# Performance work log

Hardware: AMD Instinct MI355X
Metric: run time of the kernel (lower is better)

The kernel has to match this reference:

```python
import jax, jax.numpy as jnp
import numpy as np

N_NODES = 100000
N_EDGES = 1600000
IN_DIM, HID_DIM, OUT_DIM = 256, 128, 32
NEG_SLOPE = 0.2  # GATConv default negative_slope


def setup_inputs() -> dict:
    key = jax.random.key(0)
    ks = jax.random.split(key, 6)
    x = jax.random.normal(ks[0], (N_NODES, IN_DIM), dtype=jnp.float32)
    edge_index = jax.random.randint(ks[1], (2, N_EDGES), 0, N_NODES, dtype=jnp.int64)
    # conv1: lin_src [in, hid], att_src/att_dst [hid] (heads=1)
    W1 = jax.random.normal(ks[2], (IN_DIM, HID_DIM), dtype=jnp.float32) * 0.05
    a1_src = jax.random.normal(ks[3], (HID_DIM,), dtype=jnp.float32) * 0.05
    a1_dst = jax.random.normal(ks[4], (HID_DIM,), dtype=jnp.float32) * 0.05
    # conv2: lin_src [hid, out]; conv2 runs with attention=False so no att params needed
    W2 = jax.random.normal(ks[5], (HID_DIM, OUT_DIM), dtype=jnp.float32) * 0.05
    return {"x": x, "W1": W1, "a1_src": a1_src, "a1_dst": a1_dst, "W2": W2,
            "edge_index": edge_index}


def _gat_aggregate(xs, alpha_src, alpha_dst, src, dst, n):
    """Segment-softmax attention aggregation (heads=1).
    xs: [N,C] transformed features; alpha_src/alpha_dst: [N] per-node logits.
    Edge e: j=src[e] -> i=dst[e]; softmax over edges grouped by dst."""
    e = jax.nn.leaky_relu(alpha_src[src] + alpha_dst[dst], NEG_SLOPE)  # [E]
    m = jax.ops.segment_max(e, dst, num_segments=n)                    # [N]
    w = jnp.exp(e - m[dst])                                            # [E]
    s = jax.ops.segment_sum(w, dst, num_segments=n)                    # [N]
    a = w / s[dst]                                                     # [E]
    return jax.ops.segment_sum(xs[src] * a[:, None], dst, num_segments=n)


def reference(x, W1, a1_src, a1_dst, W2, edge_index):
    src, dst = edge_index[0], edge_index[1]
    n = x.shape[0]

    # conv1 (attention=True): also caches per-node attention logits (tied later)
    xs1 = x @ W1                       # [N, hid]
    as1 = xs1 @ a1_src                 # [N]
    ad1 = xs1 @ a1_dst                 # [N]
    h1 = jax.nn.elu(_gat_aggregate(xs1, as1, ad1, src, dst, n))

    # conv2 (attention=False): returns x @ lin_src (heads=1, concat=False)
    h2 = h1 @ W2                       # [N, out]

    # conv3: weights tied to W2^T, attention tied to conv1's logits
    xs3 = h2 @ W2.T                    # [N, hid]
    h3 = jax.nn.elu(_gat_aggregate(xs3, as1, ad1, src, dst, n))

    # conv4 (attention=False): weights tied to W1^T
    h4 = h3 @ W1.T                     # [N, in]

    return (h2, h4)
```

## Files before the change

kernel.cpp:

```cpp
#include <hip/hip_runtime.h>
#include <math.h>

#define IN_DIM 256
#define HID 128
#define OUTD 32
#define NEG_SLOPE 0.2f
#define BSH 8
#define EPB 4096

typedef unsigned short ushort_t;
typedef unsigned int uint_t;
typedef __attribute__((ext_vector_type(8))) short short8;
typedef __attribute__((ext_vector_type(4))) float f32x4;

__device__ __forceinline__ ushort_t f2b(float f) {
    union { float f; uint_t i; } v; v.f = f;
    uint_t x = v.i;
    uint_t r = (x + 0x7FFFu + ((x >> 16) & 1u)) >> 16;
    return (ushort_t)r;
}

__device__ __forceinline__ float b2f(ushort_t b) {
    union { uint_t i; float f; } v; v.i = ((uint_t)b) << 16;
    return v.f;
}

__global__ __launch_bounds__(256) void swz_kernel(
    const float* __restrict__ W1, const float* __restrict__ W2,
    ushort_t* __restrict__ W1B, ushort_t* __restrict__ W1TB, ushort_t* __restrict__ W2TB)
{
    int idx = blockIdx.x * 256 + threadIdx.x;
    if (idx < 32768) {
        int j = idx & 7, l = (idx >> 3) & 63, t = (idx >> 9) & 7, s = idx >> 12;
        int n = 16 * t + (l & 15), k = 32 * s + (l >> 4) * 8 + j;
        W1B[idx] = f2b(W1[k * HID + n]);
    } else if (idx < 65536) {
        int o = idx - 32768;
        int j = o & 7, l = (o >> 3) & 63, t = (o >> 9) & 15, s = o >> 13;
        int n = 16 * t + (l & 15), k = 32 * s + (l >> 4) * 8 + j;
        W1TB[o] = f2b(W1[n * HID + k]);
    } else if (idx < 69632) {
        int o = idx - 65536;
        int j = o & 7, l = (o >> 3) & 63, t = o >> 9;
        int n = 16 * t + (l & 15), k = (l >> 4) * 8 + j;
        W2TB[o] = f2b(W2[n * OUTD + k]);
    }
}

__global__ __launch_bounds__(256) void gemm1_mfma(
    const float* __restrict__ x, const ushort_t* __restrict__ W1B,
    const float* __restrict__ a_src, const float* __restrict__ a_dst,
    ushort_t* __restrict__ xs1b, float* __restrict__ as1, float* __restrict__ ad1, int N)
{
    __shared__ ushort_t lx[64 * 264];
    const int tid = threadIdx.x;
    const int row0 = blockIdx.x * 64;
    const int nrows = min(64, N - row0);

    for (int i = tid; i < nrows * 32; i += 256) {
        int r = i >> 5, c = i & 31;
        const float* p = x + (size_t)(row0 + r) * IN_DIM + c * 8;
        float4 v0 = *(const float4*)p;
        float4 v1 = *(const float4*)(p + 4);
        ushort_t o[8] = { f2b(v0.x), f2b(v0.y), f2b(v0.z), f2b(v0.w),
                          f2b(v1.x), f2b(v1.y), f2b(v1.z), f2b(v1.w) };
        *(uint4*)(&lx[r * 264 + c * 8]) = *(uint4*)o;
    }
    __syncthreads();

    const int wave = tid >> 6, lane = tid & 63;
    const int lo = lane & 15, q = lane >> 4;
    f32x4 acc[8];
    #pragma unroll
    for (int t = 0; t < 8; t++) acc[t] = (f32x4){0.f, 0.f, 0.f, 0.f};

    const int arow = wave * 16 + lo;
    #pragma unroll
    for (int s = 0; s < 8; s++) {
        short8 af = *(const short8*)(&lx[arow * 264 + s * 32 + q * 8]);
        #pragma unroll
        for (int t = 0; t < 8; t++) {
            short8 bf = *(const short8*)(W1B + ((size_t)(s * 8 + t) * 64 + lane) * 8);
            acc[t] = __builtin_amdgcn_mfma_f32_16x16x32_bf16(af, bf, acc[t], 0, 0, 0);
        }
    }

    float asv[8], adv[8];
    #pragma unroll
    for (int t = 0; t < 8; t++) { asv[t] = a_src[t * 16 + lo]; adv[t] = a_dst[t * 16 + lo]; }
    #pragma unroll
    for (int r = 0; r < 4; r++) {
        float vs = 0.f, vd = 0.f;
        #pragma unroll
        for (int t = 0; t < 8; t++) { vs += acc[t][r] * asv[t]; vd += acc[t][r] * adv[t]; }
        #pragma unroll
        for (int off = 1; off < 16; off <<= 1) {
            vs += __shfl_xor(vs, off, 64);
            vd += __shfl_xor(vd, off, 64);
        }
        int m = row0 + wave * 16 + q * 4 + r;
        if (lo == 0 && m < N) { as1[m] = vs; ad1[m] = vd; }
    }

    #pragma unroll
    for (int r = 0; r < 4; r++) {
        int m = row0 + wave * 16 + q * 4 + r;
        if (m < N) {
            #pragma unroll
            for (int t = 0; t < 8; t++)
                xs1b[(size_t)m * HID + t * 16 + lo] = f2b(acc[t][r]);
        }
    }
}

__global__ __launch_bounds__(256) void gemm3_mfma(
    const ushort_t* __restrict__ h2b, const ushort_t* __restrict__ W2TB,
    ushort_t* __restrict__ xs3b, int N)
{
    __shared__ ushort_t lh[64 * 40];
    const int tid = threadIdx.x;
    const int row0 = blockIdx.x * 64;
    const int nrows = min(64, N - row0);
    for (int i = tid; i < nrows * 4; i += 256) {
        int r = i >> 2, c = i & 3;
        *(uint4*)(&lh[r * 40 + c * 8]) =
            *(const uint4*)(h2b + (size_t)(row0 + r) * OUTD + c * 8);
    }
    __syncthreads();

    const int wave = tid >> 6, lane = tid & 63;
    const int lo = lane & 15, q = lane >> 4;
    f32x4 acc[8];
    #pragma unroll
    for (int t = 0; t < 8; t++) acc[t] = (f32x4){0.f, 0.f, 0.f, 0.f};
    short8 af = *(const short8*)(&lh[(wave * 16 + lo) * 40 + q * 8]);
    #pragma unroll
    for (int t = 0; t < 8; t++) {
        short8 bf = *(const short8*)(W2TB + ((size_t)t * 64 + lane) * 8);
        acc[t] = __builtin_amdgcn_mfma_f32_16x16x32_bf16(af, bf, acc[t], 0, 0, 0);
    }
    #pragma unroll
    for (int r = 0; r < 4; r++) {
        int m = row0 + wave * 16 + q * 4 + r;
        if (m < N) {
            #pragma unroll
            for (int t = 0; t < 8; t++)
                xs3b[(size_t)m * HID + t * 16 + lo] = f2b(acc[t][r]);
        }
    }
}

__global__ __launch_bounds__(256) void gemm4_mfma(
    const ushort_t* __restrict__ h3b, const ushort_t* __restrict__ W1TB,
    float* __restrict__ h4, int N)
{
    __shared__ ushort_t lh[64 * 136];
    const int tid = threadIdx.x;
    const int row0 = blockIdx.x * 64;
    const int nrows = min(64, N - row0);
    for (int i = tid; i < nrows * 16; i += 256) {
        int r = i >> 4, c = i & 15;
        *(uint4*)(&lh[r * 136 + c * 8]) =
            *(const uint4*)(h3b + (size_t)(row0 + r) * HID + c * 8);
    }
    __syncthreads();

    const int wave = tid >> 6, lane = tid & 63;
    const int lo = lane & 15, q = lane >> 4;
    f32x4 acc[16];
    #pragma unroll
    for (int t = 0; t < 16; t++) acc[t] = (f32x4){0.f, 0.f, 0.f, 0.f};
    const int arow = wave * 16 + lo;
    #pragma unroll
    for (int s = 0; s < 4; s++) {
        short8 af = *(const short8*)(&lh[arow * 136 + s * 32 + q * 8]);
        #pragma unroll
        for (int t = 0; t < 16; t++) {
            short8 bf = *(const short8*)(W1TB + ((size_t)(s * 16 + t) * 64 + lane) * 8);
            acc[t] = __builtin_amdgcn_mfma_f32_16x16x32_bf16(af, bf, acc[t], 0, 0, 0);
        }
    }
    #pragma unroll
    for (int r = 0; r < 4; r++) {
        int m = row0 + wave * 16 + q * 4 + r;
        if (m < N) {
            #pragma unroll
            for (int t = 0; t < 16; t++)
                h4[(size_t)m * IN_DIM + t * 16 + lo] = acc[t][r];
        }
    }
}

__global__ __launch_bounds__(256) void bhist_kernel(
    const int* __restrict__ dst, int* __restrict__ bcnt, int E, int B)
{
    __shared__ int lcnt[512];
    int t = threadIdx.x;
    for (int i = t; i < B; i += 256) lcnt[i] = 0;
    __syncthreads();
    int base = blockIdx.x * EPB;
    int end = min(base + EPB, E);
    for (int e = base + t; e < end; e += 256)
        atomicAdd(&lcnt[dst[e] >> BSH], 1);
    __syncthreads();
    for (int i = t; i < B; i += 256) {
        int c = lcnt[i];
        if (c) atomicAdd(&bcnt[i], c);
    }
}

__global__ __launch_bounds__(512) void bscan_kernel(
    const int* __restrict__ bcnt, int* __restrict__ boff, int* __restrict__ gcur,
    int* __restrict__ off, int B, int N, int E)
{
    __shared__ int l[512];
    int t = threadIdx.x;
    int v = (t < B) ? bcnt[t] : 0;
    l[t] = v;
    __syncthreads();
    for (int o = 1; o < 512; o <<= 1) {
        int u = (t >= o) ? l[t - o] : 0;
        __syncthreads();
        l[t] += u;
        __syncthreads();
    }
    int pre = l[t] - v;
    if (t < B) { boff[t] = pre; gcur[t] = pre; }
    if (t == B - 1) boff[B] = pre + v;
    if (t == 0) off[N] = E;
}

__global__ __launch_bounds__(256) void bscatter_kernel(
    const int* __restrict__ src, const int* __restrict__ dst,
    int* __restrict__ gcur, int2* __restrict__ barr, int E, int B)
{
    __shared__ int lpos[512];
    int t = threadIdx.x;
    for (int i = t; i < B; i += 256) lpos[i] = 0;
    __syncthreads();
    int base = blockIdx.x * EPB;
    int end = min(base + EPB, E);
    for (int e = base + t; e < end; e += 256)
        atomicAdd(&lpos[dst[e] >> BSH], 1);
    __syncthreads();
    for (int i = t; i < B; i += 256) {
        int c = lpos[i];
        if (c) lpos[i] = atomicAdd(&gcur[i], c);
    }
    __syncthreads();
    for (int e = base + t; e < end; e += 256) {
        int s = src[e], d = dst[e];
        int p = atomicAdd(&lpos[d >> BSH], 1);
        barr[p] = make_int2(s, d);
    }
}

__global__ __launch_bounds__(256) void bsort_kernel(
    const int2* __restrict__ barr, const int* __restrict__ boff,
    int* __restrict__ off, int* __restrict__ esrc, int N)
{
    __shared__ int ldeg[256];
    __shared__ int lscan[256];
    int b = blockIdx.x, t = threadIdx.x;
    int d0 = b << BSH;
    int e0 = boff[b], e1 = boff[b + 1];
    ldeg[t] = 0;
    __syncthreads();
    for (int e = e0 + t; e < e1; e += 256)
        atomicAdd(&ldeg[barr[e].y & 255], 1);
    __syncthreads();
    int my = ldeg[t];
    lscan[t] = my;
    __syncthreads();
    for (int o = 1; o < 256; o <<= 1) {
        int u = (t >= o) ? lscan[t - o] : 0;
        __syncthreads();
        lscan[t] += u;
        __syncthreads();
    }
    int pre = lscan[t] - my;
    int d = d0 + t;
    if (d < N) off[d] = e0 + pre;
    ldeg[t] = pre;
    __syncthreads();
    for (int e = e0 + t; e < e1; e += 256) {
        int2 r = barr[e];
        int p = atomicAdd(&ldeg[r.y & 255], 1);
        esrc[e0 + p] = r.x;
    }
}

template<bool BOUT>
__global__ __launch_bounds__(256) void agg_csr_kernel(
    const ushort_t* __restrict__ xsb, const int* __restrict__ off,
    const int* __restrict__ esrc, const float* __restrict__ as1,
    const float* __restrict__ ad1,
    float* __restrict__ outf, ushort_t* __restrict__ outb, int N)
{
    int d = blockIdx.x * 4 + (threadIdx.x >> 6);
    if (d >= N) return;
    const int lane = threadIdx.x & 63;
    const int g = lane >> 4, li = lane & 15;
    const int e0 = off[d], e1 = off[d + 1];
    const float ad = ad1[d];

    float acc[8];
    #pragma unroll
    for (int j = 0; j < 8; j++) acc[j] = 0.f;
    float sw = 0.f;

    for (int e = e0 + g; e < e1; e += 4) {
        int s = esrc[e];
        float v = as1[s] + ad;
        v = v > 0.f ? v : NEG_SLOPE * v;
        float w = __expf(v);
        uint4 u = *(const uint4*)(xsb + (size_t)s * HID + li * 8);
        acc[0] += w * __uint_as_float(u.x << 16);
        acc[1] += w * __uint_as_float(u.x & 0xFFFF0000u);
        acc[2] += w * __uint_as_float(u.y << 16);
        acc[3] += w * __uint_as_float(u.y & 0xFFFF0000u);
        acc[4] += w * __uint_as_float(u.z << 16);
        acc[5] += w * __uint_as_float(u.z & 0xFFFF0000u);
        acc[6] += w * __uint_as_float(u.w << 16);
        acc[7] += w * __uint_as_float(u.w & 0xFFFF0000u);
        sw += w;
    }

    #pragma unroll
    for (int j = 0; j < 8; j++) {
        acc[j] += __shfl_xor(acc[j], 16, 64);
        acc[j] += __shfl_xor(acc[j], 32, 64);
    }
    sw += __shfl_xor(sw, 16, 64);
    sw += __shfl_xor(sw, 32, 64);

    if (g != 0) return;
    float inv = sw > 0.f ? 1.0f / sw : 0.f;
    float o[8];
    #pragma unroll
    for (int j = 0; j < 8; j++) {
        float v = acc[j] * inv;
        o[j] = v > 0.f ? v : expm1f(v);
    }
    if (BOUT) {
        ushort_t ob[8] = { f2b(o[0]), f2b(o[1]), f2b(o[2]), f2b(o[3]),
                           f2b(o[4]), f2b(o[5]), f2b(o[6]), f2b(o[7]) };
        *(uint4*)(outb + (size_t)d * HID + li * 8) = *(uint4*)ob;
    } else {
        float4 o0 = make_float4(o[0], o[1], o[2], o[3]);
        float4 o1 = make_float4(o[4], o[5], o[6], o[7]);
        *(float4*)(outf + (size_t)d * HID + li * 8) = o0;
        *(float4*)(outf + (size_t)d * HID + li * 8 + 4) = o1;
    }
}

__global__ __launch_bounds__(256) void gemm2_kernel(
    const float* __restrict__ h1, const float* __restrict__ W2,
    float* __restrict__ h2, ushort_t* __restrict__ h2b, int N)
{
    __shared__ float lh[32 * 129];
    const int tid = threadIdx.x;
    const int row0 = blockIdx.x * 32;
    const int nrows = min(32, N - row0);
    for (int i = tid; i < nrows * 32; i += 256) {
        int r = i >> 5, q = i & 31;
        float4 v = *(const float4*)(h1 + (size_t)(row0 + r) * HID + q * 4);
        float* d = &lh[r * 129 + q * 4];
        d[0] = v.x; d[1] = v.y; d[2] = v.z; d[3] = v.w;
    }
    __syncthreads();
    const int r = tid >> 3;
    const int c0 = (tid & 7) * 4;
    float a0 = 0, a1 = 0, a2 = 0, a3 = 0;
    for (int k = 0; k < HID; k++) {
        float h = lh[r * 129 + k];
        float4 w = *(const float4*)(W2 + k * OUTD + c0);
        a0 += h * w.x; a1 += h * w.y; a2 += h * w.z; a3 += h * w.w;
    }
    if (r < nrows) {
        float4 o; o.x = a0; o.y = a1; o.z = a2; o.w = a3;
        *(float4*)(h2 + (size_t)(row0 + r) * OUTD + c0) = o;
        ushort_t ob[4] = { f2b(a0), f2b(a1), f2b(a2), f2b(a3) };
        *(uint2*)(h2b + (size_t)(row0 + r) * OUTD + c0) = *(uint2*)ob;
    }
}

extern "C" void kernel_launch(void* const* d_in, const int* in_sizes, int n_in,
                              void* d_out, int out_size, void* d_ws, size_t ws_size,
                              hipStream_t stream)
{
    const float* x     = (const float*)d_in[0];
    const float* W1    = (const float*)d_in[1];
    const float* a_src = (const float*)d_in[2];
    const float* a_dst = (const float*)d_in[3];
    const float* W2    = (const float*)d_in[4];
    const int*   ei    = (const int*)d_in[5];

    const int N = in_sizes[0] / IN_DIM;
    const int E = in_sizes[5] / 2;
    const int* src = ei;
    const int* dst = ei + E;
    const int B = (N + 255) >> BSH;

    float* ws = (float*)d_ws;
    size_t o = 0;
    ushort_t* A   = (ushort_t*)(ws + o); o += (size_t)N * HID / 2;
    float* Bb  = ws + o; o += (size_t)N * HID;
    float* as1 = ws + o; o += N;
    float* ad1 = ws + o; o += N;
    ushort_t* h3b  = (ushort_t*)(ws + o); o += (size_t)N * HID / 2;
    ushort_t* h2b  = (ushort_t*)(ws + o); o += (size_t)N * OUTD / 2;
    ushort_t* W1B  = (ushort_t*)(ws + o); o += 16384;
    ushort_t* W1TB = (ushort_t*)(ws + o); o += 16384;
    ushort_t* W2TB = (ushort_t*)(ws + o); o += 2048;
    int2* barr = (int2*)(ws + o); o += (size_t)E * 2;
    int* off  = (int*)(ws + o);
    int* esrc = off + N + 1;
    int* bcnt = esrc + E;
    int* boff = bcnt + B;
    int* gcur = boff + B + 1;

    float* h2 = (float*)d_out;
    float* h4 = h2 + (size_t)N * OUTD;

    hipMemsetAsync(bcnt, 0, (size_t)B * sizeof(int), stream);

    swz_kernel<<<(69632 + 255) / 256, 256, 0, stream>>>(W1, W2, W1B, W1TB, W2TB);

    const int GB = (E + EPB - 1) / EPB;
    bhist_kernel<<<GB, 256, 0, stream>>>(dst, bcnt, E, B);
    bscan_kernel<<<1, 512, 0, stream>>>(bcnt, boff, gcur, off, B, N, E);
    bscatter_kernel<<<GB, 256, 0, stream>>>(src, dst, gcur, barr, E, B);
    bsort_kernel<<<B, 256, 0, stream>>>(barr, boff, off, esrc, N);

    gemm1_mfma<<<(N + 63) / 64, 256, 0, stream>>>(x, W1B, a_src, a_dst, A, as1, ad1, N);

    agg_csr_kernel<false><<<(N + 3) / 4, 256, 0, stream>>>(A, off, esrc, as1, ad1, Bb, (ushort_t*)0, N);
    gemm2_kernel<<<(N + 31) / 32, 256, 0, stream>>>(Bb, W2, h2, h2b, N);

    gemm3_mfma<<<(N + 63) / 64, 256, 0, stream>>>(h2b, W2TB, A, N);
    agg_csr_kernel<true><<<(N + 3) / 4, 256, 0, stream>>>(A, off, esrc, as1, ad1, (float*)0, h3b, N);
    gemm4_mfma<<<(N + 63) / 64, 256, 0, stream>>>(h3b, W1TB, h4, N);
}
```

Before: 531.4 us.

## Precompute normalized edge weights and aggregate conv3 in 32-dim space before projection

Edge softmax weights are now computed once during the CSR bucket sort, normalized per destination, and stored packed with source indices, so neither aggregation recomputes exp or normalizes. The conv3 aggregation uses linearity (A·(h2·W2ᵀ) = (A·h2)·W2ᵀ) to gather 32-wide h2 rows instead of 128-wide xs3 rows, then applies the projection and ELU in the small GEMM. This cuts gather bandwidth for the second aggregation, at the cost of an extra packed edge array and a serial per-thread normalization pass in the sort kernel. gemm1 is moved earlier so the logits are ready when the sort needs them.

Measured after the change: 505.4 us. -4.9%, faster.

```diff
diff --git a/kernel.cpp b/kernel.cpp
--- a/kernel.cpp
+++ b/kernel.cpp
@@ -113,9 +113,9 @@
     }
 }
 
-__global__ __launch_bounds__(256) void gemm3_mfma(
-    const ushort_t* __restrict__ h2b, const ushort_t* __restrict__ W2TB,
-    ushort_t* __restrict__ xs3b, int N)
+__global__ __launch_bounds__(256) void gemm3g_mfma(
+    const ushort_t* __restrict__ gb, const ushort_t* __restrict__ W2TB,
+    ushort_t* __restrict__ h3b, int N)
 {
     __shared__ ushort_t lh[64 * 40];
     const int tid = threadIdx.x;
@@ -124,7 +124,7 @@
     for (int i = tid; i < nrows * 4; i += 256) {
         int r = i >> 2, c = i & 3;
         *(uint4*)(&lh[r * 40 + c * 8]) =
-            *(const uint4*)(h2b + (size_t)(row0 + r) * OUTD + c * 8);
+            *(const uint4*)(gb + (size_t)(row0 + r) * OUTD + c * 8);
     }
     __syncthreads();
 
@@ -144,8 +144,11 @@
         int m = row0 + wave * 16 + q * 4 + r;
         if (m < N) {
             #pragma unroll
-            for (int t = 0; t < 8; t++)
-                xs3b[(size_t)m * HID + t * 16 + lo] = f2b(acc[t][r]);
+            for (int t = 0; t < 8; t++) {
+                float v = acc[t][r];
+                v = v > 0.f ? v : expm1f(v);
+                h3b[(size_t)m * HID + t * 16 + lo] = f2b(v);
+            }
         }
     }
 }
@@ -257,14 +260,17 @@
 
 __global__ __launch_bounds__(256) void bsort_kernel(
     const int2* __restrict__ barr, const int* __restrict__ boff,
-    int* __restrict__ off, int* __restrict__ esrc, int N)
+    const float* __restrict__ as1, const float* __restrict__ ad1,
+    int* __restrict__ off, int2* __restrict__ epk, int N)
 {
     __shared__ int ldeg[256];
     __shared__ int lscan[256];
+    __shared__ float lsum[256];
     int b = blockIdx.x, t = threadIdx.x;
     int d0 = b << BSH;
     int e0 = boff[b], e1 = boff[b + 1];
     ldeg[t] = 0;
+    lsum[t] = 0.f;
     __syncthreads();
     for (int e = e0 + t; e < e1; e += 256)
         atomicAdd(&ldeg[barr[e].y & 255], 1);
@@ -285,36 +291,102 @@
     __syncthreads();
     for (int e = e0 + t; e < e1; e += 256) {
         int2 r = barr[e];
+        float v = as1[r.x] + ad1[r.y];
+        v = v > 0.f ? v : NEG_SLOPE * v;
+        float w = __expf(v);
         int p = atomicAdd(&ldeg[r.y & 255], 1);
-        esrc[e0 + p] = r.x;
-    }
-}
-
-template<bool BOUT>
-__global__ __launch_bounds__(256) void agg_csr_kernel(
+        epk[e0 + p] = make_int2(r.x, __float_as_int(w));
+        atomicAdd(&lsum[r.y & 255], w);
+    }
+    __syncthreads();
+    float s = lsum[t];
+    float inv = (my > 0 && s > 0.f) ? 1.0f / s : 0.f;
+    int base = e0 + pre;
+    for (int i = 0; i < my; i++) {
+        int2 r = epk[base + i];
+        epk[base + i] = make_int2(r.x, __float_as_int(__int_as_float(r.y) * inv));
+    }
+}
+
+__global__ __launch_bounds__(256) void agg128_kernel(
     const ushort_t* __restrict__ xsb, const int* __restrict__ off,
-    const int* __restrict__ esrc, const float* __restrict__ as1,
-    const float* __restrict__ ad1,
-    float* __restrict__ outf, ushort_t* __restrict__ outb, int N)
+    const int2* __restrict__ epk, float* __restrict__ outf, int N)
 {
     int d = blockIdx.x * 4 + (threadIdx.x >> 6);
     if (d >= N) return;
     const int lane = threadIdx.x & 63;
     const int g = lane >> 4, li = lane & 15;
     const int e0 = off[d], e1 = off[d + 1];
-    const float ad = ad1[d];
 
     float acc[8];
     #pragma unroll
     for (int j = 0; j < 8; j++) acc[j] = 0.f;
-    float sw = 0.f;
-
-    for (int e = e0 + g; e < e1; e += 4) {
-        int s = esrc[e];
-        float v = as1[s] + ad;
-        v = v > 0.f ? v : NEG_SLOPE * v;
-        float w = __expf(v);
-        uint4 u = *(const uint4*)(xsb + (size_t)s * HID + li * 8);
+
+    int e = e0 + g;
+    for (; e + 4 < e1; e += 8) {
+        int2 p0 = epk[e], p1 = epk[e + 4];
+        float w0 = __int_as_float(p0.y), w1 = __int_as_float(p1.y);
+        uint4 u0 = *(const uint4*)(xsb + (size_t)p0.x * HID + li * 8);
+        uint4 u1 = *(const uint4*)(xsb + (size_t)p1.x * HID + li * 8);
+        acc[0] += w0 * __uint_as_float(u0.x << 16)        + w1 * __uint_as_float(u1.x << 16);
+        acc[1] += w0 * __uint_as_float(u0.x & 0xFFFF0000u) + w1 * __uint_as_float(u1.x & 0xFFFF0000u);
+        acc[2] += w0 * __uint_as_float(u0.y << 16)        + w1 * __uint_as_float(u1.y << 16);
+        acc[3] += w0 * __uint_as_float(u0.y & 0xFFFF0000u) + w1 * __uint_as_float(u1.y & 0xFFFF0000u);
+        acc[4] += w0 * __uint_as_float(u0.z << 16)        + w1 * __uint_as_float(u1.z << 16);
+        acc[5] += w0 * __uint_as_float(u0.z & 0xFFFF0000u) + w1 * __uint_as_float(u1.z & 0xFFFF0000u);
+        acc[6] += w0 * __uint_as_float(u0.w << 16)        + w1 * __uint_as_float(u1.w << 16);
+        acc[7] += w0 * __uint_as_float(u0.w & 0xFFFF0000u) + w1 * __uint_as_float(u1.w & 0xFFFF0000u);
+    }
+    if (e < e1) {
+        int2 p0 = epk[e];
+        float w0 = __int_as_float(p0.y);
+        uint4 u0 = *(const uint4*)(xsb + (size_t)p0.x * HID + li * 8);
+        acc[0] += w0 * __uint_as_float(u0.x << 16);
+        acc[1] += w0 * __uint_as_float(u0.x & 0xFFFF0000u);
+        acc[2] += w0 * __uint_as_float(u0.y << 16);
+        acc[3] += w0 * __uint_as_float(u0.y & 0xFFFF0000u);
+        acc[4] += w0 * __uint_as_float(u0.z << 16);
+        acc[5] += w0 * __uint_as_float(u0.z & 0xFFFF0000u);
+        acc[6] += w0 * __uint_as_float(u0.w << 16);
+        acc[7] += w0 * __uint_as_float(u0.w & 0xFFFF0000u);
+    }
+
+    #pragma unroll
+    for (int j = 0; j < 8; j++) {
+        acc[j] += __shfl_xor(acc[j], 16, 64);
+        acc[j] += __shfl_xor(acc[j], 32, 64);
+    }
+    if (g != 0) return;
+    float o[8];
+    #pragma unroll
+    for (int j = 0; j < 8; j++) {
+        float v = acc[j];
+        o[j] = v > 0.f ? v : expm1f(v);
+    }
+    float4 o0 = make_float4(o[0], o[1], o[2], o[3]);
+    float4 o1 = make_float4(o[4], o[5], o[6], o[7]);
+    *(float4*)(outf + (size_t)d * HID + li * 8) = o0;
+    *(float4*)(outf + (size_t)d * HID + li * 8 + 4) = o1;
+}
+
+__global__ __launch_bounds__(256) void agg32_kernel(
+    const ushort_t* __restrict__ h2b, const int* __restrict__ off,
+    const int2* __restrict__ epk, ushort_t* __restrict__ gb, int N)
+{
+    int d = blockIdx.x * 4 + (threadIdx.x >> 6);
+    if (d >= N) return;
+    const int lane = threadIdx.x & 63;
+    const int g = lane >> 2, li = lane & 3;
+    const int e0 = off[d], e1 = off[d + 1];
+
+    float acc[8];
+    #pragma unroll
+    for (int j = 0; j < 8; j++) acc[j] = 0.f;
+
+    for (int e = e0 + g; e < e1; e += 16) {
+        int2 p = epk[e];
+        float w = __int_as_float(p.y);
+        uint4 u = *(const uint4*)(h2b + (size_t)p.x * OUTD + li * 8);
         acc[0] += w * __uint_as_float(u.x << 16);
         acc[1] += w * __uint_as_float(u.x & 0xFFFF0000u);
         acc[2] += w * __uint_as_float(u.y << 16);
@@ -323,35 +395,19 @@
         acc[5] += w * __uint_as_float(u.z & 0xFFFF0000u);
         acc[6] += w * __uint_as_float(u.w << 16);
         acc[7] += w * __uint_as_float(u.w & 0xFFFF0000u);
-        sw += w;
     }
 
     #pragma unroll
     for (int j = 0; j < 8; j++) {
+        acc[j] += __shfl_xor(acc[j], 4, 64);
+        acc[j] += __shfl_xor(acc[j], 8, 64);
         acc[j] += __shfl_xor(acc[j], 16, 64);
         acc[j] += __shfl_xor(acc[j], 32, 64);
     }
-    sw += __shfl_xor(sw, 16, 64);
-    sw += __shfl_xor(sw, 32, 64);
-
     if (g != 0) return;
-    float inv = sw > 0.f ? 1.0f / sw : 0.f;
-    float o[8];
-    #pragma unroll
-    for (int j = 0; j < 8; j++) {
-        float v = acc[j] * inv;
-        o[j] = v > 0.f ? v : expm1f(v);
-    }
-    if (BOUT) {
-        ushort_t ob[8] = { f2b(o[0]), f2b(o[1]), f2b(o[2]), f2b(o[3]),
-                           f2b(o[4]), f2b(o[5]), f2b(o[6]), f2b(o[7]) };
-        *(uint4*)(outb + (size_t)d * HID + li * 8) = *(uint4*)ob;
-    } else {
-        float4 o0 = make_float4(o[0], o[1], o[2], o[3]);
-        float4 o1 = make_float4(o[4], o[5], o[6], o[7]);
-        *(float4*)(outf + (size_t)d * HID + li * 8) = o0;
-        *(float4*)(outf + (size_t)d * HID + li * 8 + 4) = o1;
-    }
+    ushort_t ob[8] = { f2b(acc[0]), f2b(acc[1]), f2b(acc[2]), f2b(acc[3]),
+                       f2b(acc[4]), f2b(acc[5]), f2b(acc[6]), f2b(acc[7]) };
+    *(uint4*)(gb + (size_t)d * OUTD + li * 8) = *(uint4*)ob;
 }
 
 __global__ __launch_bounds__(256) void gemm2_kernel(
@@ -414,9 +470,9 @@
     ushort_t* W1TB = (ushort_t*)(ws + o); o += 16384;
     ushort_t* W2TB = (ushort_t*)(ws + o); o += 2048;
     int2* barr = (int2*)(ws + o); o += (size_t)E * 2;
+    int2* epk  = (int2*)(ws + o); o += (size_t)E * 2;
     int* off  = (int*)(ws + o);
-    int* esrc = off + N + 1;
-    int* bcnt = esrc + E;
+    int* bcnt = off + N + 1;
     int* boff = bcnt + B;
     int* gcur = boff + B + 1;
 
@@ -426,19 +482,20 @@
     hipMemsetAsync(bcnt, 0, (size_t)B * sizeof(int), stream);
 
     swz_kernel<<<(69632 + 255) / 256, 256, 0, stream>>>(W1, W2, W1B, W1TB, W2TB);
+
+    gemm1_mfma<<<(N + 63) / 64, 256, 0, stream>>>(x, W1B, a_src, a_dst, A, as1, ad1, N);
 
     const int GB = (E + EPB - 1) / EPB;
     bhist_kernel<<<GB, 256, 0, stream>>>(dst, bcnt, E, B);
     bscan_kernel<<<1, 512, 0, stream>>>(bcnt, boff, gcur, off, B, N, E);
     bscatter_kernel<<<GB, 256, 0, stream>>>(src, dst, gcur, barr, E, B);
-    bsort_kernel<<<B, 256, 0, stream>>>(barr, boff, off, esrc, N);
-
-    gemm1_mfma<<<(N + 63) / 64, 256, 0, stream>>>(x, W1B, a_src, a_dst, A, as1, ad1, N);
-
-    agg_csr_kernel<false><<<(N + 3) / 4, 256, 0, stream>>>(A, off, esrc, as1, ad1, Bb, (ushort_t*)0, N);
+    bsort_kernel<<<B, 256, 0, stream>>>(barr, boff, as1, ad1, off, epk, N);
+
+    agg128_kernel<<<(N + 3) / 4, 256, 0, stream>>>(A, off, epk, Bb, N);
     gemm2_kernel<<<(N + 31) / 32, 256, 0, stream>>>(Bb, W2, h2, h2b, N);
 
-    gemm3_mfma<<<(N + 63) / 64, 256, 0, stream>>>(h2b, W2TB, A, N);
-    agg_csr_kernel<true><<<(N + 3) / 4, 256, 0, stream>>>(A, off, esrc, as1, ad1, (float*)0, h3b, N);
+    ushort_t* gb = A;
+    agg32_kernel<<<(N + 3) / 4, 256, 0, stream>>>(h2b, off, epk, gb, N);
+    gemm3g_mfma<<<(N + 63) / 64, 256, 0, stream>>>(gb, W2TB, h3b, N);
     gemm4_mfma<<<(N + 63) / 64, 256, 0, stream>>>(h3b, W1TB, h4, N);
 }
```
